# Kernel tuning notes

Measured on AMD Instinct MI355X. Metric: run time of the kernel, lower is better.

## Reference

```python
import jax, jax.numpy as jnp
import numpy as np

N_NODES = 10000


def gcn_conv(x, W, b, src, dst, num_nodes):
    """PyG GCNConv: add self-loops, symmetric deg^{-1/2} normalization,
    linear transform (no bias in lin), scatter-add aggregation, then bias."""
    xw = x @ W  # (N, H)
    # degree on A + I (self-loops added)
    deg = jnp.zeros((num_nodes,), dtype=x.dtype).at[dst].add(1.0) + 1.0
    dinv = jax.lax.rsqrt(deg)  # (N,)
    norm = dinv[src] * dinv[dst]  # (E,)
    msg = xw[src] * norm[:, None]  # (E, H) gathered messages
    agg = jax.ops.segment_sum(msg, dst, num_segments=num_nodes)
    # self-loop contribution: norm_ii = dinv_i^2
    agg = agg + xw * (dinv * dinv)[:, None]
    return agg + b


def setup_inputs() -> dict:
    key = jax.random.key(0)
    k1, k2, k3, k4 = jax.random.split(key, 4)
    N, F, H, E = N_NODES, 256, 512, 320000
    x = jax.random.normal(k1, (N, F), dtype=jnp.float32)
    edge_index = jax.random.randint(k2, (2, E), 0, N, dtype=jnp.int64)
    W1 = jax.random.normal(k3, (F, H), dtype=jnp.float32) * (1.0 / np.sqrt(F))
    b1 = jnp.zeros((H,), dtype=jnp.float32)
    W2 = jax.random.normal(k4, (H, F), dtype=jnp.float32) * (1.0 / np.sqrt(H))
    b2 = jnp.zeros((F,), dtype=jnp.float32)
    return {"x": x, "edge_index": edge_index, "W1": W1, "b1": b1, "W2": W2, "b2": b2}


def reference(x, edge_index, W1, b1, W2, b2):
    src, dst = edge_index[0], edge_index[1]
    h = jax.nn.relu(gcn_conv(x, W1, b1, src, dst, N_NODES))
    h = jax.nn.relu(gcn_conv(h, W2, b2, src, dst, N_NODES))
    # global_max_pool with single graph (batch all zeros) -> (1, F)
    return jnp.max(h, axis=0, keepdims=True)
```

## Files before the change

### kernel.cpp

```cpp
#include <hip/hip_runtime.h>

#define NNODES 10000
#define MP 10112
#define F 256
#define H 512
#define CAP 128
#define H1STR 520
#define ZROW NNODES

typedef _Float16 half8 __attribute__((ext_vector_type(8)));
typedef float floatx4 __attribute__((ext_vector_type(4)));
typedef float floatx8 __attribute__((ext_vector_type(8)));
typedef int intx4 __attribute__((ext_vector_type(4)));

__global__ __launch_bounds__(256) void build_k(const int* __restrict__ src,
                                               const int* __restrict__ dst,
                                               int* __restrict__ cnt,
                                               int* __restrict__ csr,
                                               const float* __restrict__ W1,
                                               const float* __restrict__ W2,
                                               _Float16* __restrict__ W1t,
                                               _Float16* __restrict__ W2t,
                                               const float* __restrict__ x,
                                               _Float16* __restrict__ xh, int E) {
  int gt = blockIdx.x * 256 + threadIdx.x;
  if (gt < E) {
    int d = dst[gt];
    int p = atomicAdd(&cnt[d], 1);
    if (p < CAP) csr[(size_t)d * CAP + p] = src[gt];
  }
  if (gt < H * F) {
    W1t[gt] = (_Float16)W1[(gt & 255) * H + (gt >> 8)];
    W2t[gt] = (_Float16)W2[(gt & 511) * F + (gt >> 9)];
  }
  if (gt < NNODES * F / 8) {
    floatx8 v = *(const floatx8*)(x + (size_t)gt * 8);
    *(half8*)(xh + (size_t)gt * 8) = __builtin_convertvector(v, half8);
  }
  if (gt < F / 8) {
    half8 z = {};
    *(half8*)(xh + (size_t)ZROW * F + (size_t)gt * 8) = z;
  }
}

template <bool WEIGHTED, bool FUSE_MAX>
__global__ __launch_bounds__(256) void aggb_k(const _Float16* __restrict__ in,
                                              const int* __restrict__ cnt,
                                              const int* __restrict__ csr,
                                              const float* __restrict__ bias,
                                              _Float16* __restrict__ outh,
                                              float* __restrict__ out) {
  __shared__ int buck[8 * CAP];
  __shared__ float wts[8 * CAP];
  __shared__ float smem[2048];
  int tid = threadIdx.x;
  int lane = tid & 63, wvi = tid >> 6;
  int half = lane >> 5, hl = lane & 31;
  int f0 = hl * 8;
  int lanebyte = hl * 16;
  int hw = wvi * 2 + half;
  int node = (blockIdx.x * 4 + wvi) * 2 + half;
  int* lb = buck + hw * CAP;
  float* wb = wts + hw * CAP;
  float one = 1.0f;
  asm("" : "+v"(one));
  floatx8 bb = {};
  if (FUSE_MAX) bb = *(const floatx8*)(bias + f0);

  int degf = cnt[node];
  int deg = min(degf, CAP);
  float di = rsqrtf((float)(degf + 1));

  intx4 bv = *(const intx4*)(csr + (size_t)node * CAP + hl * 4);
  if (WEIGHTED) {
    int e0 = hl * 4;
    int idx[4];
    #pragma unroll
    for (int j = 0; j < 4; j++) idx[j] = (e0 + j < deg) ? bv[j] : node;
    int cv[4];
    #pragma unroll
    for (int j = 0; j < 4; j++) cv[j] = cnt[idx[j]];
    intx4 ov; floatx4 wv;
    #pragma unroll
    for (int j = 0; j < 4; j++) {
      bool valid = (e0 + j) < deg;
      ov[j] = (valid ? bv[j] : ZROW) << 9;
      wv[j] = valid ? rsqrtf((float)(cv[j] + 1)) : 0.f;
    }
    *(intx4*)(lb + hl * 4) = ov;
    *(floatx4*)(wb + hl * 4) = wv;
  } else {
    #pragma unroll
    for (int j = 0; j < 4; j++) bv[j] <<= 9;
    *(intx4*)(lb + hl * 4) = bv;
    int degp0 = (deg + 15) & ~15;
    if (hl < degp0 - deg) lb[deg + hl] = ZROW << 9;
  }
  int degp = (deg + 15) & ~15;

  const char* inb = (const char*)in;
  half8 xsv = *(const half8*)(in + (size_t)node * F + f0);
  floatx8 acc;
  if (WEIGHTED) {
    #pragma unroll
    for (int t = 0; t < 8; t++) acc[t] = 0.f;
  } else {
    #pragma unroll
    for (int t = 0; t < 8; t++) acc[t] = (float)xsv[t];
  }

  for (int c = 0; c < degp; c += 16) {
    intx4 iv[4];
    floatx4 wq[4];
    #pragma unroll
    for (int j = 0; j < 4; j++) iv[j] = *(const intx4*)(lb + c + j * 4);
    if (WEIGHTED)
      #pragma unroll
      for (int j = 0; j < 4; j++) wq[j] = *(const floatx4*)(wb + c + j * 4);
    half8 hv[16];
    #pragma unroll
    for (int j = 0; j < 4; j++)
      #pragma unroll
      for (int k = 0; k < 4; k++)
        hv[j * 4 + k] = *(const half8*)(inb + (iv[j][k] + lanebyte));
    #pragma unroll
    for (int j = 0; j < 4; j++)
      #pragma unroll
      for (int k = 0; k < 4; k++) {
        float w = WEIGHTED ? wq[j][k] : one;
        #pragma unroll
        for (int t = 0; t < 8; t++)
          acc[t] = __builtin_fmaf((float)hv[j * 4 + k][t], w, acc[t]);
      }
  }

  if (FUSE_MAX) {
    floatx8 lm;
    #pragma unroll
    for (int t = 0; t < 8; t++) lm[t] = fmaxf(di * acc[t] + bb[t], 0.f);
    *(floatx8*)(smem + hw * 256 + f0) = lm;
    __syncthreads();
    float m = smem[tid];
    #pragma unroll
    for (int r = 1; r < 8; r++) m = fmaxf(m, smem[r * 256 + tid]);
    atomicMax((int*)&out[tid], __float_as_int(m));
  } else {
    float d2 = di * di;
    floatx8 tot;
    #pragma unroll
    for (int t = 0; t < 8; t++)
      tot[t] = di * acc[t] + d2 * (float)xsv[t];
    *(half8*)(outh + (size_t)node * F + f0) = __builtin_convertvector(tot, half8);
  }
}

__global__ __launch_bounds__(256) void gemm12_k(const _Float16* __restrict__ A,
                                                const _Float16* __restrict__ W1t,
                                                const float* __restrict__ b1,
                                                const _Float16* __restrict__ W2t,
                                                const int* __restrict__ cnt,
                                                _Float16* __restrict__ C) {
  __shared__ _Float16 h1[32 * H1STR];
  int lane = threadIdx.x & 63;
  int wv = threadIdx.x >> 6;
  int r = lane & 15, q = lane >> 4;
  int m0 = blockIdx.x * 32;

  {
    floatx4 acc[2][8] = {};
    const _Float16* Ap = A + (size_t)(m0 + r) * F + q * 8;
    const _Float16* Bp = W1t + (size_t)(wv * 128 + r) * F + q * 8;
    for (int k0 = 0; k0 < F; k0 += 32) {
      half8 a[2], b[8];
      #pragma unroll
      for (int i = 0; i < 2; i++) a[i] = *(const half8*)(Ap + (size_t)i * 16 * F + k0);
      #pragma unroll
      for (int j = 0; j < 8; j++) b[j] = *(const half8*)(Bp + (size_t)j * 16 * F + k0);
      #pragma unroll
      for (int i = 0; i < 2; i++)
        #pragma unroll
        for (int j = 0; j < 8; j++)
          acc[i][j] = __builtin_amdgcn_mfma_f32_16x16x32_f16(a[i], b[j], acc[i][j], 0, 0, 0);
    }
    #pragma unroll
    for (int i = 0; i < 2; i++) {
      #pragma unroll
      for (int j = 0; j < 8; j++) {
        int n = wv * 128 + j * 16 + r;
        float bv = b1[n];
        #pragma unroll
        for (int rr = 0; rr < 4; rr++) {
          int row = i * 16 + q * 4 + rr;
          h1[row * H1STR + n] = (_Float16)fmaxf(acc[i][j][rr] + bv, 0.f);
        }
      }
    }
  }
  __syncthreads();

  {
    float sc[2][4];
    #pragma unroll
    for (int i = 0; i < 2; i++)
      #pragma unroll
      for (int rr = 0; rr < 4; rr++) {
        int row = m0 + i * 16 + q * 4 + rr;
        sc[i][rr] = (row < NNODES) ? rsqrtf((float)(cnt[row] + 1)) : 0.f;
      }
    floatx4 acc[2][4] = {};
    const _Float16* Bp = W2t + (size_t)(wv * 64 + r) * H + q * 8;
    for (int k0 = 0; k0 < H; k0 += 32) {
      half8 a[2], b[4];
      #pragma unroll
      for (int i = 0; i < 2; i++)
        a[i] = *(const half8*)(h1 + (i * 16 + r) * H1STR + k0 + q * 8);
      #pragma unroll
      for (int j = 0; j < 4; j++) b[j] = *(const half8*)(Bp + (size_t)j * 16 * H + k0);
      #pragma unroll
      for (int i = 0; i < 2; i++)
        #pragma unroll
        for (int j = 0; j < 4; j++)
          acc[i][j] = __builtin_amdgcn_mfma_f32_16x16x32_f16(a[i], b[j], acc[i][j], 0, 0, 0);
    }
    #pragma unroll
    for (int i = 0; i < 2; i++) {
      #pragma unroll
      for (int j = 0; j < 4; j++) {
        int n = wv * 64 + j * 16 + r;
        #pragma unroll
        for (int rr = 0; rr < 4; rr++) {
          int row = m0 + i * 16 + q * 4 + rr;
          float val = (row < NNODES) ? acc[i][j][rr] * sc[i][rr] : 0.f;
          C[(size_t)row * F + n] = (_Float16)val;
        }
      }
    }
  }
}

extern "C" void kernel_launch(void* const* d_in, const int* in_sizes, int n_in,
                              void* d_out, int out_size, void* d_ws, size_t ws_size,
                              hipStream_t stream) {
  const float* x  = (const float*)d_in[0];
  const int*   ei = (const int*)d_in[1];
  const float* W1 = (const float*)d_in[2];
  const float* b1 = (const float*)d_in[3];
  const float* W2 = (const float*)d_in[4];
  const float* b2 = (const float*)d_in[5];
  const int E = in_sizes[1] / 2;
  const int N = NNODES;
  const int* src = ei;
  const int* dst = ei + E;

  char* w = (char*)d_ws;
  size_t off = 0;
  auto take = [&](size_t bytes) -> void* {
    void* p = w + off;
    off += (bytes + 255) & ~(size_t)255;
    return p;
  };
  int*       cnt    = (int*)take((size_t)N * 4);
  int*       csr    = (int*)take((size_t)N * CAP * 4);
  _Float16*  W1t    = (_Float16*)take((size_t)H * F * 2);
  _Float16*  W2t    = (_Float16*)take((size_t)F * H * 2);
  _Float16*  xh     = (_Float16*)take((size_t)(N + 1) * F * 2);
  _Float16*  axh    = (_Float16*)take((size_t)MP * F * 2);
  _Float16*  xw2h   = (_Float16*)take((size_t)MP * F * 2);

  hipMemsetAsync(cnt, 0, (size_t)N * 4, stream);
  build_k<<<1250, 256, 0, stream>>>(src, dst, cnt, csr, W1, W2, W1t, W2t, x, xh, E);
  aggb_k<true, false><<<1250, 256, 0, stream>>>(xh, cnt, csr, nullptr, axh, nullptr);
  gemm12_k<<<MP / 32, 256, 0, stream>>>(axh, W1t, b1, W2t, cnt, xw2h);
  aggb_k<false, true><<<1250, 256, 0, stream>>>(xw2h, cnt, csr, b2, nullptr, (float*)d_out);
}
```

Measured before the change: 177.7 us.

## Fuse all GCN stages into one persistent cooperative kernel with grid syncs

Replaces the four separate launches (build, weighted aggregation, fused GEMM, aggregation with max) with a single cooperative mega-kernel. Grid-wide barriers separate the stages, and blocks grid-stride over the work in each one. The aim is to remove inter-kernel launch gaps and tail drain. In exchange it adds grid-sync cost, caps the grid at occupancy-limited persistent blocks, and shares LDS through a union, which may lower occupancy and balance in the aggregation phases.

```diff
diff --git a/kernel.cpp b/kernel.cpp
--- a/kernel.cpp
+++ b/kernel.cpp
@@ -1,4 +1,7 @@
 #include <hip/hip_runtime.h>
+#include <hip/hip_cooperative_groups.h>
+
+namespace cg = cooperative_groups;
 
 #define NNODES 10000
 #define MP 10112
@@ -7,233 +10,255 @@
 #define CAP 128
 #define H1STR 520
 #define ZROW NNODES
+#define NTILES (MP / 32)
 
 typedef _Float16 half8 __attribute__((ext_vector_type(8)));
 typedef float floatx4 __attribute__((ext_vector_type(4)));
 typedef float floatx8 __attribute__((ext_vector_type(8)));
 typedef int intx4 __attribute__((ext_vector_type(4)));
 
-__global__ __launch_bounds__(256) void build_k(const int* __restrict__ src,
-                                               const int* __restrict__ dst,
-                                               int* __restrict__ cnt,
-                                               int* __restrict__ csr,
-                                               const float* __restrict__ W1,
-                                               const float* __restrict__ W2,
-                                               _Float16* __restrict__ W1t,
-                                               _Float16* __restrict__ W2t,
-                                               const float* __restrict__ x,
-                                               _Float16* __restrict__ xh, int E) {
-  int gt = blockIdx.x * 256 + threadIdx.x;
-  if (gt < E) {
-    int d = dst[gt];
-    int p = atomicAdd(&cnt[d], 1);
-    if (p < CAP) csr[(size_t)d * CAP + p] = src[gt];
-  }
-  if (gt < H * F) {
-    W1t[gt] = (_Float16)W1[(gt & 255) * H + (gt >> 8)];
-    W2t[gt] = (_Float16)W2[(gt & 511) * F + (gt >> 9)];
-  }
-  if (gt < NNODES * F / 8) {
-    floatx8 v = *(const floatx8*)(x + (size_t)gt * 8);
-    *(half8*)(xh + (size_t)gt * 8) = __builtin_convertvector(v, half8);
-  }
-  if (gt < F / 8) {
-    half8 z = {};
-    *(half8*)(xh + (size_t)ZROW * F + (size_t)gt * 8) = z;
-  }
-}
+struct LdsAgg {
+  int buck[8 * CAP];
+  float wts[8 * CAP];
+  float red[2048];
+};
+union LdsU {
+  LdsAgg agg;
+  _Float16 h1[32 * H1STR];
+};
 
 template <bool WEIGHTED, bool FUSE_MAX>
-__global__ __launch_bounds__(256) void aggb_k(const _Float16* __restrict__ in,
-                                              const int* __restrict__ cnt,
-                                              const int* __restrict__ csr,
-                                              const float* __restrict__ bias,
-                                              _Float16* __restrict__ outh,
-                                              float* __restrict__ out) {
-  __shared__ int buck[8 * CAP];
-  __shared__ float wts[8 * CAP];
-  __shared__ float smem[2048];
-  int tid = threadIdx.x;
+__device__ __forceinline__ void agg_do(const _Float16* __restrict__ in,
+                                       const int* __restrict__ cnt,
+                                       const int* __restrict__ csr,
+                                       const float* __restrict__ bias,
+                                       _Float16* __restrict__ outh,
+                                       float* __restrict__ out,
+                                       LdsAgg* S, int node, int tid) {
   int lane = tid & 63, wvi = tid >> 6;
   int half = lane >> 5, hl = lane & 31;
-  int f0 = hl * 8;
-  int lanebyte = hl * 16;
   int hw = wvi * 2 + half;
-  int node = (blockIdx.x * 4 + wvi) * 2 + half;
-  int* lb = buck + hw * CAP;
-  float* wb = wts + hw * CAP;
+  int f0 = hl * 8, lanebyte = hl * 16;
+  int* lb = S->buck + hw * CAP;
+  float* wb = S->wts + hw * CAP;
   float one = 1.0f;
   asm("" : "+v"(one));
-  floatx8 bb = {};
-  if (FUSE_MAX) bb = *(const floatx8*)(bias + f0);
-
-  int degf = cnt[node];
-  int deg = min(degf, CAP);
-  float di = rsqrtf((float)(degf + 1));
-
-  intx4 bv = *(const intx4*)(csr + (size_t)node * CAP + hl * 4);
-  if (WEIGHTED) {
-    int e0 = hl * 4;
-    int idx[4];
+  bool vn = (node < NNODES);
+  float di = 0.f;
+  floatx8 acc = {};
+  half8 xsv = {};
+  if (vn) {
+    int degf = cnt[node];
+    int deg = min(degf, CAP);
+    di = rsqrtf((float)(degf + 1));
+    intx4 bv = *(const intx4*)(csr + (size_t)node * CAP + hl * 4);
+    if (WEIGHTED) {
+      int e0 = hl * 4;
+      int idx[4];
+      #pragma unroll
+      for (int j = 0; j < 4; j++) idx[j] = (e0 + j < deg) ? bv[j] : node;
+      int cv[4];
+      #pragma unroll
+      for (int j = 0; j < 4; j++) cv[j] = cnt[idx[j]];
+      intx4 ov; floatx4 wv;
+      #pragma unroll
+      for (int j = 0; j < 4; j++) {
+        bool valid = (e0 + j) < deg;
+        ov[j] = (valid ? bv[j] : ZROW) << 9;
+        wv[j] = valid ? rsqrtf((float)(cv[j] + 1)) : 0.f;
+      }
+      *(intx4*)(lb + hl * 4) = ov;
+      *(floatx4*)(wb + hl * 4) = wv;
+    } else {
+      #pragma unroll
+      for (int j = 0; j < 4; j++) bv[j] <<= 9;
+      *(intx4*)(lb + hl * 4) = bv;
+      int degp0 = (deg + 15) & ~15;
+      if (hl < degp0 - deg) lb[deg + hl] = ZROW << 9;
+    }
+    int degp = (deg + 15) & ~15;
+    const char* inb = (const char*)in;
+    xsv = *(const half8*)(in + (size_t)node * F + f0);
+    if (!WEIGHTED) {
+      #pragma unroll
+      for (int t = 0; t < 8; t++) acc[t] = (float)xsv[t];
+    }
+    for (int c = 0; c < degp; c += 16) {
+      intx4 iv[4]; floatx4 wq[4];
+      #pragma unroll
+      for (int j = 0; j < 4; j++) iv[j] = *(const intx4*)(lb + c + j * 4);
+      if (WEIGHTED)
+        #pragma unroll
+        for (int j = 0; j < 4; j++) wq[j] = *(const floatx4*)(wb + c + j * 4);
+      half8 hv[16];
+      #pragma unroll
+      for (int j = 0; j < 4; j++)
+        #pragma unroll
+        for (int k = 0; k < 4; k++)
+          hv[j * 4 + k] = *(const half8*)(inb + (iv[j][k] + lanebyte));
+      #pragma unroll
+      for (int j = 0; j < 4; j++)
+        #pragma unroll
+        for (int k = 0; k < 4; k++) {
+          float wgt = WEIGHTED ? wq[j][k] : one;
+          #pragma unroll
+          for (int t = 0; t < 8; t++)
+            acc[t] = __builtin_fmaf((float)hv[j * 4 + k][t], wgt, acc[t]);
+        }
+    }
+  }
+  if (FUSE_MAX) {
+    floatx8 lm = {};
+    if (vn) {
+      floatx8 bb = *(const floatx8*)(bias + f0);
+      #pragma unroll
+      for (int t = 0; t < 8; t++) lm[t] = fmaxf(di * acc[t] + bb[t], 0.f);
+    }
+    *(floatx8*)(S->red + hw * 256 + f0) = lm;
+    __syncthreads();
+    float m = S->red[tid];
     #pragma unroll
-    for (int j = 0; j < 4; j++) idx[j] = (e0 + j < deg) ? bv[j] : node;
-    int cv[4];
-    #pragma unroll
-    for (int j = 0; j < 4; j++) cv[j] = cnt[idx[j]];
-    intx4 ov; floatx4 wv;
-    #pragma unroll
-    for (int j = 0; j < 4; j++) {
-      bool valid = (e0 + j) < deg;
-      ov[j] = (valid ? bv[j] : ZROW) << 9;
-      wv[j] = valid ? rsqrtf((float)(cv[j] + 1)) : 0.f;
-    }
-    *(intx4*)(lb + hl * 4) = ov;
-    *(floatx4*)(wb + hl * 4) = wv;
-  } else {
-    #pragma unroll
-    for (int j = 0; j < 4; j++) bv[j] <<= 9;
-    *(intx4*)(lb + hl * 4) = bv;
-    int degp0 = (deg + 15) & ~15;
-    if (hl < degp0 - deg) lb[deg + hl] = ZROW << 9;
-  }
-  int degp = (deg + 15) & ~15;
-
-  const char* inb = (const char*)in;
-  half8 xsv = *(const half8*)(in + (size_t)node * F + f0);
-  floatx8 acc;
-  if (WEIGHTED) {
-    #pragma unroll
-    for (int t = 0; t < 8; t++) acc[t] = 0.f;
-  } else {
-    #pragma unroll
-    for (int t = 0; t < 8; t++) acc[t] = (float)xsv[t];
-  }
-
-  for (int c = 0; c < degp; c += 16) {
-    intx4 iv[4];
-    floatx4 wq[4];
-    #pragma unroll
-    for (int j = 0; j < 4; j++) iv[j] = *(const intx4*)(lb + c + j * 4);
-    if (WEIGHTED)
-      #pragma unroll
-      for (int j = 0; j < 4; j++) wq[j] = *(const floatx4*)(wb + c + j * 4);
-    half8 hv[16];
-    #pragma unroll
-    for (int j = 0; j < 4; j++)
-      #pragma unroll
-      for (int k = 0; k < 4; k++)
-        hv[j * 4 + k] = *(const half8*)(inb + (iv[j][k] + lanebyte));
-    #pragma unroll
-    for (int j = 0; j < 4; j++)
-      #pragma unroll
-      for (int k = 0; k < 4; k++) {
-        float w = WEIGHTED ? wq[j][k] : one;
-        #pragma unroll
-        for (int t = 0; t < 8; t++)
-          acc[t] = __builtin_fmaf((float)hv[j * 4 + k][t], w, acc[t]);
-      }
-  }
-
-  if (FUSE_MAX) {
-    floatx8 lm;
-    #pragma unroll
-    for (int t = 0; t < 8; t++) lm[t] = fmaxf(di * acc[t] + bb[t], 0.f);
-    *(floatx8*)(smem + hw * 256 + f0) = lm;
+    for (int r = 1; r < 8; r++) m = fmaxf(m, S->red[r * 256 + tid]);
+    atomicMax((int*)&out[tid], __float_as_int(m));
     __syncthreads();
-    float m = smem[tid];
-    #pragma unroll
-    for (int r = 1; r < 8; r++) m = fmaxf(m, smem[r * 256 + tid]);
-    atomicMax((int*)&out[tid], __float_as_int(m));
-  } else {
+  } else if (vn) {
     float d2 = di * di;
     floatx8 tot;
     #pragma unroll
     for (int t = 0; t < 8; t++)
-      tot[t] = di * acc[t] + d2 * (float)xsv[t];
+      tot[t] = WEIGHTED ? (di * acc[t] + d2 * (float)xsv[t]) : (di * acc[t]);
     *(half8*)(outh + (size_t)node * F + f0) = __builtin_convertvector(tot, half8);
   }
 }
 
-__global__ __launch_bounds__(256) void gemm12_k(const _Float16* __restrict__ A,
-                                                const _Float16* __restrict__ W1t,
-                                                const float* __restrict__ b1,
-                                                const _Float16* __restrict__ W2t,
-                                                const int* __restrict__ cnt,
-                                                _Float16* __restrict__ C) {
-  __shared__ _Float16 h1[32 * H1STR];
-  int lane = threadIdx.x & 63;
-  int wv = threadIdx.x >> 6;
-  int r = lane & 15, q = lane >> 4;
-  int m0 = blockIdx.x * 32;
+__global__ __launch_bounds__(256, 4) void mega_k(
+    const float* __restrict__ x, const int* __restrict__ srcp,
+    const int* __restrict__ dstp, const float* __restrict__ W1,
+    const float* __restrict__ b1, const float* __restrict__ W2,
+    const float* __restrict__ b2, int* __restrict__ cnt,
+    int* __restrict__ csr, _Float16* __restrict__ W1t,
+    _Float16* __restrict__ W2t, _Float16* __restrict__ xh,
+    _Float16* __restrict__ axh, _Float16* __restrict__ xw2h,
+    float* __restrict__ out, int E) {
+  __shared__ LdsU L;
+  cg::grid_group gg = cg::this_grid();
+  int tid = threadIdx.x, bid = blockIdx.x, nblk = gridDim.x;
+  int GS = nblk * 256;
+  int gt = bid * 256 + tid;
+
+  for (int g = gt; g < H * F; g += GS) {
+    W1t[g] = (_Float16)W1[(g & 255) * H + (g >> 8)];
+    W2t[g] = (_Float16)W2[(g & 511) * F + (g >> 9)];
+  }
+  for (int g = gt; g < NNODES * F / 8; g += GS) {
+    floatx8 v = *(const floatx8*)(x + (size_t)g * 8);
+    *(half8*)(xh + (size_t)g * 8) = __builtin_convertvector(v, half8);
+  }
+  if (gt < F / 8) {
+    half8 z = {};
+    *(half8*)(xh + (size_t)ZROW * F + (size_t)gt * 8) = z;
+  }
+  for (int g = gt; g < E; g += GS) {
+    int d = dstp[g];
+    int p = atomicAdd(&cnt[d], 1);
+    if (p < CAP) csr[(size_t)d * CAP + p] = srcp[g];
+  }
+  __threadfence();
+  gg.sync();
 
   {
-    floatx4 acc[2][8] = {};
-    const _Float16* Ap = A + (size_t)(m0 + r) * F + q * 8;
-    const _Float16* Bp = W1t + (size_t)(wv * 128 + r) * F + q * 8;
-    for (int k0 = 0; k0 < F; k0 += 32) {
-      half8 a[2], b[8];
-      #pragma unroll
-      for (int i = 0; i < 2; i++) a[i] = *(const half8*)(Ap + (size_t)i * 16 * F + k0);
-      #pragma unroll
-      for (int j = 0; j < 8; j++) b[j] = *(const half8*)(Bp + (size_t)j * 16 * F + k0);
+    int per = nblk * 8;
+    for (int nb0 = 0; nb0 < NNODES; nb0 += per) {
+      int node = nb0 + bid * 8 + (tid >> 6) * 2 + ((tid & 63) >> 5);
+      agg_do<true, false>(xh, cnt, csr, nullptr, axh, nullptr, &L.agg, node, tid);
+    }
+  }
+  __threadfence();
+  gg.sync();
+
+  for (int t = bid; t < NTILES; t += nblk) {
+    int lane = tid & 63, wv = tid >> 6;
+    int r = lane & 15, q = lane >> 4;
+    int m0 = t * 32;
+    {
+      floatx4 acc[2][8] = {};
+      const _Float16* Ap = axh + (size_t)(m0 + r) * F + q * 8;
+      const _Float16* Bp = W1t + (size_t)(wv * 128 + r) * F + q * 8;
+      for (int k0 = 0; k0 < F; k0 += 32) {
+        half8 a[2], b[8];
+        #pragma unroll
+        for (int i = 0; i < 2; i++) a[i] = *(const half8*)(Ap + (size_t)i * 16 * F + k0);
+        #pragma unroll
+        for (int j = 0; j < 8; j++) b[j] = *(const half8*)(Bp + (size_t)j * 16 * F + k0);
+        #pragma unroll
+        for (int i = 0; i < 2; i++)
+          #pragma unroll
+          for (int j = 0; j < 8; j++)
+            acc[i][j] = __builtin_amdgcn_mfma_f32_16x16x32_f16(a[i], b[j], acc[i][j], 0, 0, 0);
+      }
+      #pragma unroll
+      for (int i = 0; i < 2; i++) {
+        #pragma unroll
+        for (int j = 0; j < 8; j++) {
+          int n = wv * 128 + j * 16 + r;
+          float bv = b1[n];
+          #pragma unroll
+          for (int rr = 0; rr < 4; rr++) {
+            int row = i * 16 + q * 4 + rr;
+            L.h1[row * H1STR + n] = (_Float16)fmaxf(acc[i][j][rr] + bv, 0.f);
+          }
+        }
+      }
+    }
+    __syncthreads();
+    {
+      float sc[2][4];
       #pragma unroll
       for (int i = 0; i < 2; i++)
-        #pragma unroll
-        for (int j = 0; j < 8; j++)
-          acc[i][j] = __builtin_amdgcn_mfma_f32_16x16x32_f16(a[i], b[j], acc[i][j], 0, 0, 0);
-    }
-    #pragma unroll
-    for (int i = 0; i < 2; i++) {
-      #pragma unroll
-      for (int j = 0; j < 8; j++) {
-        int n = wv * 128 + j * 16 + r;
-        float bv = b1[n];
-        #pragma unroll
-        for (int rr = 0; rr < 4; rr++) {
-          int row = i * 16 + q * 4 + rr;
-          h1[row * H1STR + n] = (_Float16)fmaxf(acc[i][j][rr] + bv, 0.f);
-        }
-      }
-    }
-  }
-  __syncthreads();
-
-  {
-    float sc[2][4];
-    #pragma unroll
-    for (int i = 0; i < 2; i++)
-      #pragma unroll
-      for (int rr = 0; rr < 4; rr++) {
-        int row = m0 + i * 16 + q * 4 + rr;
-        sc[i][rr] = (row < NNODES) ? rsqrtf((float)(cnt[row] + 1)) : 0.f;
-      }
-    floatx4 acc[2][4] = {};
-    const _Float16* Bp = W2t + (size_t)(wv * 64 + r) * H + q * 8;
-    for (int k0 = 0; k0 < H; k0 += 32) {
-      half8 a[2], b[4];
-      #pragma unroll
-      for (int i = 0; i < 2; i++)
-        a[i] = *(const half8*)(h1 + (i * 16 + r) * H1STR + k0 + q * 8);
-      #pragma unroll
-      for (int j = 0; j < 4; j++) b[j] = *(const half8*)(Bp + (size_t)j * 16 * H + k0);
-      #pragma unroll
-      for (int i = 0; i < 2; i++)
-        #pragma unroll
-        for (int j = 0; j < 4; j++)
-          acc[i][j] = __builtin_amdgcn_mfma_f32_16x16x32_f16(a[i], b[j], acc[i][j], 0, 0, 0);
-    }
-    #pragma unroll
-    for (int i = 0; i < 2; i++) {
-      #pragma unroll
-      for (int j = 0; j < 4; j++) {
-        int n = wv * 64 + j * 16 + r;
         #pragma unroll
         for (int rr = 0; rr < 4; rr++) {
           int row = m0 + i * 16 + q * 4 + rr;
-          float val = (row < NNODES) ? acc[i][j][rr] * sc[i][rr] : 0.f;
-          C[(size_t)row * F + n] = (_Float16)val;
+          sc[i][rr] = (row < NNODES) ? rsqrtf((float)(cnt[row] + 1)) : 0.f;
         }
-      }
+      floatx4 acc[2][4] = {};
+      const _Float16* Bp = W2t + (size_t)(wv * 64 + r) * H + q * 8;
+      for (int k0 = 0; k0 < H; k0 += 32) {
+        half8 a[2], b[4];
+        #pragma unroll
+        for (int i = 0; i < 2; i++)
+          a[i] = *(const half8*)(L.h1 + (i * 16 + r) * H1STR + k0 + q * 8);
+        #pragma unroll
+        for (int j = 0; j < 4; j++) b[j] = *(const half8*)(Bp + (size_t)j * 16 * H + k0);
+        #pragma unroll
+        for (int i = 0; i < 2; i++)
+          #pragma unroll
+          for (int j = 0; j < 4; j++)
+            acc[i][j] = __builtin_amdgcn_mfma_f32_16x16x32_f16(a[i], b[j], acc[i][j], 0, 0, 0);
+      }
+      #pragma unroll
+      for (int i = 0; i < 2; i++) {
+        #pragma unroll
+        for (int j = 0; j < 4; j++) {
+          int n = wv * 64 + j * 16 + r;
+          #pragma unroll
+          for (int rr = 0; rr < 4; rr++) {
+            int row = m0 + i * 16 + q * 4 + rr;
+            float val = (row < NNODES) ? acc[i][j][rr] * sc[i][rr] : 0.f;
+            xw2h[(size_t)row * F + n] = (_Float16)val;
+          }
+        }
+      }
+    }
+    __syncthreads();
+  }
+  __threadfence();
+  gg.sync();
+
+  {
+    int per = nblk * 8;
+    for (int nb0 = 0; nb0 < NNODES; nb0 += per) {
+      int node = nb0 + bid * 8 + (tid >> 6) * 2 + ((tid & 63) >> 5);
+      agg_do<false, true>(xw2h, cnt, csr, b2, nullptr, out, &L.agg, node, tid);
     }
   }
 }
@@ -266,10 +291,21 @@
   _Float16*  xh     = (_Float16*)take((size_t)(N + 1) * F * 2);
   _Float16*  axh    = (_Float16*)take((size_t)MP * F * 2);
   _Float16*  xw2h   = (_Float16*)take((size_t)MP * F * 2);
+  float*     outp   = (float*)d_out;
+  int        Ev     = E;
 
   hipMemsetAsync(cnt, 0, (size_t)N * 4, stream);
-  build_k<<<1250, 256, 0, stream>>>(src, dst, cnt, csr, W1, W2, W1t, W2t, x, xh, E);
-  aggb_k<true, false><<<1250, 256, 0, stream>>>(xh, cnt, csr, nullptr, axh, nullptr);
-  gemm12_k<<<MP / 32, 256, 0, stream>>>(axh, W1t, b1, W2t, cnt, xw2h);
-  aggb_k<false, true><<<1250, 256, 0, stream>>>(xw2h, cnt, csr, b2, nullptr, (float*)d_out);
+
+  int nb = 0;
+  if (hipOccupancyMaxActiveBlocksPerMultiprocessor(&nb, mega_k, 256, 0) != hipSuccess || nb < 1)
+    nb = 2;
+  int grid = nb * 256;
+  if (grid > 1024) grid = 1024;
+
+  void* args[] = {(void*)&x,   (void*)&src, (void*)&dst,  (void*)&W1,
+                  (void*)&b1,  (void*)&W2,  (void*)&b2,   (void*)&cnt,
+                  (void*)&csr, (void*)&W1t, (void*)&W2t,  (void*)&xh,
+                  (void*)&axh, (void*)&xw2h,(void*)&outp, (void*)&Ev};
+  hipLaunchCooperativeKernel((const void*)mega_k, dim3(grid), dim3(256),
+                             args, 0, stream);
 }
```

Result: slower. 584.5 us (+228.9%).
